# Performance work log

Hardware: AMD Instinct MI355X
Metric: run time of the kernel (lower is better)

The kernel has to match this reference:

```python
import jax, jax.numpy as jnp
import numpy as np

VO, SO, VIN, SM = 16, 100, 16, 100
B, N, K = 2, 8192, 30
EPS = 1e-8

def _split(x, nv):
    v = x[..., :3 * nv].reshape(x.shape[:-1] + (nv, 3))
    s = x[..., 3 * nv:]
    return v, s

def _merge(v, s):
    return jnp.concatenate([v.reshape(v.shape[:-2] + (-1,)), s], axis=-1)

def _vnorm(v):  # [..., nv, 3] -> [..., nv]
    return jnp.sqrt(jnp.sum(v * v, axis=-1) + EPS)

def gvp(x, nv_in, Wh, Wv, Ws, bs, nls=True, nlv=True):
    v, s = _split(x, nv_in)
    vh = jnp.einsum('...ic,ih->...hc', v, Wh)          # vi -> h vector linear
    vn = _vnorm(vh)                                     # rotation-invariant norms
    s_out = jnp.concatenate([s, vn], axis=-1) @ Ws + bs
    if nls:
        s_out = jax.nn.relu(s_out)
    v_out = jnp.einsum('...hc,ho->...oc', vh, Wv)       # h -> vo vector linear
    if nlv:
        v_out = v_out * jax.nn.sigmoid(_vnorm(v_out))[..., None]
    return _merge(v_out, s_out)

def gvp_layernorm(x, nv, g, b):
    v, s = _split(x, nv)
    vn2 = jnp.sum(v * v, axis=-1, keepdims=True)        # [..., nv, 1]
    denom = jnp.sqrt(jnp.mean(vn2, axis=-2, keepdims=True) + EPS)
    v = v / denom
    mu = jnp.mean(s, axis=-1, keepdims=True)
    var = jnp.var(s, axis=-1, keepdims=True)
    s = (s - mu) / jnp.sqrt(var + 1e-5) * g + b
    return _merge(v, s)

def setup_inputs() -> dict:
    key = jax.random.key(0)
    ks = jax.random.split(key, 24)
    def W(i, shape):
        return jax.random.normal(ks[i], shape, dtype=jnp.float32) / np.float32(np.sqrt(shape[0]))
    d = {}
    d['h_V'] = jax.random.normal(ks[0], (B, N, 3 * VO + SO), dtype=jnp.float32)
    d['h_M'] = jax.random.normal(ks[1], (B, N, K, 3 * VIN + SM), dtype=jnp.float32)
    d['mask_V'] = jax.random.randint(ks[2], (B, N), 0, 2, dtype=jnp.int32)
    d['mask_attend'] = jax.random.randint(ks[3], (B, N, K), 0, 2, dtype=jnp.int32)
    # W_EV: GVP(vi=32,si=200,vo=16,so=100,h=32) -> GVP(16,100,16,100) -> GVP(16,100,16,100,no nl)
    d['Wh1'] = W(4, (32, 32)); d['Wv1'] = W(5, (32, 16)); d['Ws1'] = W(6, (232, 100)); d['bs1'] = jnp.zeros((100,), jnp.float32)
    d['Wh2'] = W(7, (16, 16)); d['Wv2'] = W(8, (16, 16)); d['Ws2'] = W(9, (116, 100)); d['bs2'] = jnp.zeros((100,), jnp.float32)
    d['Wh3'] = W(10, (16, 16)); d['Wv3'] = W(11, (16, 16)); d['Ws3'] = W(12, (116, 100)); d['bs3'] = jnp.zeros((100,), jnp.float32)
    # W_dh: GVP(vi=16,si=100,vo=32,so=400,h=32) -> GVP(vi=32,si=400,vo=16,so=100,h=32,no nl)
    d['Wh4'] = W(13, (16, 32)); d['Wv4'] = W(14, (32, 32)); d['Ws4'] = W(15, (132, 400)); d['bs4'] = jnp.zeros((400,), jnp.float32)
    d['Wh5'] = W(16, (32, 32)); d['Wv5'] = W(17, (32, 16)); d['Ws5'] = W(18, (432, 100)); d['bs5'] = jnp.zeros((100,), jnp.float32)
    d['ln0_g'] = jnp.ones((SO,), jnp.float32); d['ln0_b'] = jnp.zeros((SO,), jnp.float32)
    d['ln1_g'] = jnp.ones((SO,), jnp.float32); d['ln1_b'] = jnp.zeros((SO,), jnp.float32)
    return d

def reference(h_V, h_M, mask_V, mask_attend,
              Wh1, Wv1, Ws1, bs1, Wh2, Wv2, Ws2, bs2, Wh3, Wv3, Ws3, bs3,
              Wh4, Wv4, Ws4, bs4, Wh5, Wv5, Ws5, bs5,
              ln0_g, ln0_b, ln1_g, ln1_b):
    # expand node features over neighbor axis and vs_concat with messages
    hVe = jnp.broadcast_to(h_V[:, :, None, :], (B, N, K, h_V.shape[-1]))
    vV, sV = _split(hVe, VO)
    vM, sM = _split(h_M, VIN)
    h_EV = _merge(jnp.concatenate([vV, vM], axis=-2), jnp.concatenate([sV, sM], axis=-1))
    m = gvp(h_EV, VO + VIN, Wh1, Wv1, Ws1, bs1)
    m = gvp(m, VO, Wh2, Wv2, Ws2, bs2)
    m = gvp(m, VO, Wh3, Wv3, Ws3, bs3, nls=False, nlv=False)
    m = mask_attend[..., None].astype(jnp.float32) * m
    dh = jnp.mean(m, axis=2)
    h = gvp_layernorm(h_V + dh, VO, ln0_g, ln0_b)  # dropout rate 0 -> identity
    dh2 = gvp(h, VO, Wh4, Wv4, Ws4, bs4)
    dh2 = gvp(dh2, 2 * VO, Wh5, Wv5, Ws5, bs5, nls=False, nlv=False)
    h = gvp_layernorm(h + dh2, VO, ln1_g, ln1_b)
    h = mask_V[..., None].astype(jnp.float32) * h
    return h
```

## Files before the change

kernel.cpp:

```cpp
#include <hip/hip_runtime.h>

#define KK 30
#define F 148
#define NNODE 16384

typedef short bf16x8 __attribute__((ext_vector_type(8)));
typedef float f32x4v __attribute__((ext_vector_type(4)));

__device__ __forceinline__ ushort f2bf(float x) {
  unsigned u = __float_as_uint(x);
  unsigned r = (u + 0x7FFF + ((u >> 16) & 1)) >> 16;
  return (ushort)r;
}
__device__ __forceinline__ float bf2f(ushort b) { return __uint_as_float(((unsigned)b) << 16); }
__device__ __forceinline__ unsigned pk2(float x, float y) {
  return (unsigned)f2bf(x) | ((unsigned)f2bf(y) << 16);
}
__device__ __forceinline__ void bsplit(float x, ushort& h, ushort& l) {
  ushort hh = f2bf(x); h = hh; l = f2bf(x - bf2f(hh));
}

#define WS_S1B 0
#define WS_VHB (NNODE * 100)
#define WS_WSB (NNODE * 100 + NNODE * 96)
#define B1HI 0
#define B1LO 17920
#define B2HI 35840
#define B2LO 50176
#define B3HI 64512
#define B3LO 78848

__global__ void prep_weights(const float* __restrict__ Ws1, const float* __restrict__ Ws2,
                             const float* __restrict__ Ws3, ushort* __restrict__ ws) {
  int i = blockIdx.x * 256 + threadIdx.x;
  if (i < 17920) {
    int n = i / 160, k = i % 160;
    float w = (n < 100 && k < 132) ? Ws1[(100 + k) * 100 + n] : 0.f;
    ushort h, l; bsplit(w, h, l);
    ws[B1HI + i] = h; ws[B1LO + i] = l;
  } else if (i < 17920 + 14336) {
    int j = i - 17920; int n = j / 128, k = j % 128;
    float w = (n < 100 && k < 116) ? Ws2[k * 100 + n] : 0.f;
    ushort h, l; bsplit(w, h, l);
    ws[B2HI + j] = h; ws[B2LO + j] = l;
  } else if (i < 17920 + 2 * 14336) {
    int j = i - 17920 - 14336; int n = j / 128, k = j % 128;
    float w = (n < 100 && k < 116) ? Ws3[k * 100 + n] : 0.f;
    ushort h, l; bsplit(w, h, l);
    ws[B3HI + j] = h; ws[B3LO + j] = l;
  }
}

__global__ __launch_bounds__(192)
void prep_node(const float* __restrict__ h_V, const float* __restrict__ Ws1,
               const float* __restrict__ bs1, const float* __restrict__ Wh1,
               float* __restrict__ s1bg, float* __restrict__ vhbg) {
  __shared__ float sv[148];
  const int node = blockIdx.x, tid = threadIdx.x;
  for (int f = tid; f < F; f += 192) sv[f] = h_V[(long)node * F + f];
  __syncthreads();
  if (tid < 100) {
    float acc = bs1[tid];
#pragma unroll 4
    for (int i = 0; i < 100; i++) acc = fmaf(sv[48 + i], Ws1[i * 100 + tid], acc);
    s1bg[node * 100 + tid] = acc;
  } else if (tid < 132) {
    int h = tid - 100;
    float a0 = 0.f, a1 = 0.f, a2 = 0.f;
#pragma unroll 4
    for (int i = 0; i < 16; i++) {
      float w = Wh1[i * 32 + h];
      a0 = fmaf(sv[3*i], w, a0); a1 = fmaf(sv[3*i+1], w, a1); a2 = fmaf(sv[3*i+2], w, a2);
    }
    vhbg[node * 96 + 3*h + 0] = a0;
    vhbg[node * 96 + 3*h + 1] = a1;
    vhbg[node * 96 + 3*h + 2] = a2;
  }
}

#define DECL12 float a00=0,a01=0,a02=0,a10=0,a11=0,a12=0,a20=0,a21=0,a22=0,a30=0,a31=0,a32=0;
#define FMA3x4(v0_,v1_,v2_,w_) \
  a00=fmaf(v0_,w_.x,a00); a01=fmaf(v1_,w_.x,a01); a02=fmaf(v2_,w_.x,a02); \
  a10=fmaf(v0_,w_.y,a10); a11=fmaf(v1_,w_.y,a11); a12=fmaf(v2_,w_.y,a12); \
  a20=fmaf(v0_,w_.z,a20); a21=fmaf(v1_,w_.z,a21); a22=fmaf(v2_,w_.z,a22); \
  a30=fmaf(v0_,w_.w,a30); a31=fmaf(v1_,w_.w,a31); a32=fmaf(v2_,w_.w,a32);

#define GATE3(x0,x1,x2,d0,d1,d2) { float vn_=sqrtf((x0)*(x0)+(x1)*(x1)+(x2)*(x2)+1e-8f); \
  float g_=1.f/(1.f+expf(-vn_)); d0=(x0)*g_; d1=(x1)*g_; d2=(x2)*g_; }

template<int NI, bool GATEF>
__device__ __forceinline__ void vtaskb(const unsigned* __restrict__ vsrc,
                                       const float* __restrict__ wbase, int wstride,
                                       float* __restrict__ vdst)
{
  DECL12
#pragma unroll 4
  for (int h2 = 0; h2 < NI / 2; h2++) {
    unsigned d0 = vsrc[3*h2+0], d1 = vsrc[3*h2+1], d2 = vsrc[3*h2+2];
    float4 w0 = *(const float4*)(wbase + (2*h2) * wstride);
    float4 w1 = *(const float4*)(wbase + (2*h2+1) * wstride);
    float e0 = bf2f((ushort)d0), e1 = bf2f((ushort)(d0 >> 16)), e2 = bf2f((ushort)d1);
    float g0 = bf2f((ushort)(d1 >> 16)), g1 = bf2f((ushort)d2), g2 = bf2f((ushort)(d2 >> 16));
    FMA3x4(e0, e1, e2, w0)
    FMA3x4(g0, g1, g2, w1)
  }
  if (GATEF) {
    GATE3(a00,a01,a02, vdst[0],vdst[1],vdst[2])
    GATE3(a10,a11,a12, vdst[3],vdst[4],vdst[5])
    GATE3(a20,a21,a22, vdst[6],vdst[7],vdst[8])
    GATE3(a30,a31,a32, vdst[9],vdst[10],vdst[11])
  } else {
    vdst[0]=a00; vdst[1]=a01; vdst[2]=a02;  vdst[3]=a10; vdst[4]=a11; vdst[5]=a12;
    vdst[6]=a20; vdst[7]=a21; vdst[8]=a22;  vdst[9]=a30; vdst[10]=a31; vdst[11]=a32;
  }
}

template<int NI>
__device__ __forceinline__ void vhtaskb(const float* __restrict__ vsrc,
                                        const float* __restrict__ wbase, int wstride,
                                        unsigned* __restrict__ vdst_u, ushort* __restrict__ ncol)
{
  DECL12
#pragma unroll 4
  for (int h = 0; h < NI; h++) {
    float v0 = vsrc[3*h], v1 = vsrc[3*h+1], v2 = vsrc[3*h+2];
    float4 w = *(const float4*)(wbase + h * wstride);
    FMA3x4(v0, v1, v2, w)
  }
  vdst_u[0] = pk2(a00,a01); vdst_u[1] = pk2(a02,a10); vdst_u[2] = pk2(a11,a12);
  vdst_u[3] = pk2(a20,a21); vdst_u[4] = pk2(a22,a30); vdst_u[5] = pk2(a31,a32);
  float n0 = sqrtf(a00*a00+a01*a01+a02*a02 + 1e-8f);
  float n1 = sqrtf(a10*a10+a11*a11+a12*a12 + 1e-8f);
  float n2 = sqrtf(a20*a20+a21*a21+a22*a22 + 1e-8f);
  float n3 = sqrtf(a30*a30+a31*a31+a32*a32 + 1e-8f);
  unsigned* p = (unsigned*)ncol;
  p[0] = pk2(n0, n1); p[1] = pk2(n2, n3);
}

template<int NKS>
__device__ __forceinline__ void mfma_nt2(const ushort* __restrict__ A, int astr,
                                         const ushort* __restrict__ B_hi,
                                         const ushort* __restrict__ B_lo,
                                         int lane, f32x4v& c0, f32x4v& c1)
{
  int r = lane & 15, q = lane >> 4;
  const int ka = q * 8;
#pragma unroll
  for (int ks = 0; ks < NKS; ks++) {
    int ko = ka + ks * 32;
    bf16x8 a0 = *(const bf16x8*)(A + r * astr + ko);
    bf16x8 a1 = *(const bf16x8*)(A + (16 + r) * astr + ko);
    bf16x8 bh = *(const bf16x8*)(B_hi + ko);
    bf16x8 bl = *(const bf16x8*)(B_lo + ko);
    c0 = __builtin_amdgcn_mfma_f32_16x16x32_bf16(a0, bh, c0, 0, 0, 0);
    c0 = __builtin_amdgcn_mfma_f32_16x16x32_bf16(a0, bl, c0, 0, 0, 0);
    c1 = __builtin_amdgcn_mfma_f32_16x16x32_bf16(a1, bh, c1, 0, 0, 0);
    c1 = __builtin_amdgcn_mfma_f32_16x16x32_bf16(a1, bl, c1, 0, 0, 0);
  }
}

#define P_SV   0
#define P_MKB  148
#define P_VA   152
#define P_VB   1624
#define P_DH   3064
#define P_A2   3164
#define P_A    5340
#define A1S 160
#define A2S 136
#define POOL_F 7900

__global__ __launch_bounds__(256, 5)
void mpnn_fused(const float* __restrict__ h_V, const float* __restrict__ h_M,
                const int* __restrict__ mask_V, const int* __restrict__ mask_attend,
                const float* __restrict__ Wh1, const float* __restrict__ Wv1,
                const float* __restrict__ Wv2, const float* __restrict__ bs2,
                const float* __restrict__ Wv3, const float* __restrict__ bs3,
                const float* __restrict__ Wh2, const float* __restrict__ Wh3,
                const float* __restrict__ Wh4, const float* __restrict__ Wv4,
                const float* __restrict__ Ws4, const float* __restrict__ bs4,
                const float* __restrict__ Wh5, const float* __restrict__ Wv5,
                const float* __restrict__ Ws5, const float* __restrict__ bs5,
                const float* __restrict__ ln0_g, const float* __restrict__ ln0_b,
                const float* __restrict__ ln1_g, const float* __restrict__ ln1_b,
                const float* __restrict__ s1bg, const float* __restrict__ vhbg,
                const ushort* __restrict__ wsb,
                float* __restrict__ out)
{
  __shared__ float pool[POOL_F];
  float* sv   = pool + P_SV;
  float* VAp  = pool + P_VA;
  ushort* VBu = (ushort*)(pool + P_VB);
  float* dhs  = pool + P_DH;
  ushort* A1 = (ushort*)(pool + P_A);
  ushort* A2 = (ushort*)(pool + P_A2);

  const int tid = threadIdx.x;
  const int node = blockIdx.x;
  const int wave = tid >> 6, lane = tid & 63;

  for (int f = tid; f < F; f += 256) sv[f] = h_V[(long)node * F + f];
  {
    unsigned long long bal = __ballot(tid < KK && mask_attend[node * KK + tid] != 0);
    if (tid == 0) *(unsigned*)(pool + P_MKB) = (unsigned)bal;
  }
  for (int t = tid; t < 448; t += 256) {
    int r = t / 14, c2 = t % 14;
    ((unsigned*)A1)[((r * A1S + 132) >> 1) + c2] = 0;
  }
  for (int t = tid; t < 192; t += 256) {
    int r = t / 6, c2 = t % 6;
    ((unsigned*)A2)[((r * A2S + 116) >> 1) + c2] = 0;
  }
  for (int task = tid; task < KK * 37; task += 256) {
    int k = task / 37, q = task % 37;
    float4 d = *(const float4*)(h_M + ((long)node * KK + k) * F + q * 4);
    if (q < 12) {
      VAp[k * 49 + q * 4 + 0] = d.x; VAp[k * 49 + q * 4 + 1] = d.y;
      VAp[k * 49 + q * 4 + 2] = d.z; VAp[k * 49 + q * 4 + 3] = d.w;
    } else {
      int j0 = q * 4 - 48;
      unsigned* p = (unsigned*)(A1 + k * A1S + j0);
      p[0] = (unsigned)f2bf(d.x) | ((unsigned)f2bf(d.y) << 16);
      p[1] = (unsigned)f2bf(d.z) | ((unsigned)f2bf(d.w) << 16);
    }
  }
  __syncthreads();

  if (tid < 240) {
    int k = tid >> 3, h0 = (tid & 7) * 4;
    const float4* vb4 = (const float4*)(vhbg + (long)node * 96 + 3 * h0);
    float4 q0 = vb4[0], q1 = vb4[1], q2 = vb4[2];
    float a00=q0.x,a01=q0.y,a02=q0.z, a10=q0.w,a11=q1.x,a12=q1.y,
          a20=q1.z,a21=q1.w,a22=q2.x, a30=q2.y,a31=q2.z,a32=q2.w;
#pragma unroll 4
    for (int i = 0; i < 16; i++) {
      float v0 = VAp[k*49+3*i], v1 = VAp[k*49+3*i+1], v2 = VAp[k*49+3*i+2];
      float4 w = *(const float4*)(Wh1 + (16 + i) * 32 + h0);
      FMA3x4(v0, v1, v2, w)
    }
    unsigned* vb = (unsigned*)(VBu + k * 96 + 3 * h0);
    vb[0]=pk2(a00,a01); vb[1]=pk2(a02,a10); vb[2]=pk2(a11,a12);
    vb[3]=pk2(a20,a21); vb[4]=pk2(a22,a30); vb[5]=pk2(a31,a32);
    float n0 = sqrtf(a00*a00+a01*a01+a02*a02 + 1e-8f);
    float n1 = sqrtf(a10*a10+a11*a11+a12*a12 + 1e-8f);
    float n2 = sqrtf(a20*a20+a21*a21+a22*a22 + 1e-8f);
    float n3 = sqrtf(a30*a30+a31*a31+a32*a32 + 1e-8f);
    unsigned* p = (unsigned*)(A1 + k * A1S + 100 + h0);
    p[0] = pk2(n0, n1); p[1] = pk2(n2, n3);
  }
  __syncthreads();

  if (wave < 2) {
    int r = lane & 15, q = lane >> 4;
    int nt0 = (wave == 0) ? 0 : 4, nt1 = (wave == 0) ? 4 : 7;
    for (int nt = nt0; nt < nt1; nt++) {
      int n = nt * 16 + r;
      float base = (n < 100) ? s1bg[(long)node * 100 + n] : 0.f;
      f32x4v c0 = {0,0,0,0}, c1 = {0,0,0,0};
      mfma_nt2<5>(A1, A1S, wsb + B1HI + n * 160, wsb + B1LO + n * 160, lane, c0, c1);
      unsigned* dst = (unsigned*)A2;
#pragma unroll
      for (int reg = 0; reg < 4; reg++) {
        int m0 = q * 4 + reg, m1 = m0 + 16;
        unsigned hx = f2bf(fmaxf(c0[reg] + base, 0.f));
        unsigned ox = __shfl_down(hx, 1);
        unsigned hy = f2bf(fmaxf(c1[reg] + base, 0.f));
        unsigned oy = __shfl_down(hy, 1);
        if (((lane & 1) == 0) && n < 100) {
          dst[(m0 * A2S + n) >> 1] = hx | (ox << 16);
          if (m1 < 30) dst[(m1 * A2S + n) >> 1] = hy | (oy << 16);
        }
      }
    }
  } else {
    int vt = tid - 128;
    if (vt < 120) { int k = vt >> 2, o0 = (vt & 3) * 4;
      vtaskb<32, true>((const unsigned*)(VBu + k * 96), Wv1 + o0, 16, VAp + k*49 + 3*o0); }
  }
  __syncthreads();

  if (tid < 120) {
    int k = tid >> 2, h0 = (tid & 3) * 4;
    vhtaskb<16>(VAp + k*49, Wh2 + h0, 16,
                (unsigned*)(VBu + k*96 + 3*h0), A2 + k*A2S + 100 + h0);
  }
  __syncthreads();

  if (wave < 2) {
    int r = lane & 15, q = lane >> 4;
    int nt0 = (wave == 0) ? 0 : 4, nt1 = (wave == 0) ? 4 : 7;
    for (int nt = nt0; nt < nt1; nt++) {
      f32x4v c0 = {0,0,0,0}, c1 = {0,0,0,0};
      int n = nt * 16 + r;
      mfma_nt2<4>(A2, A2S, wsb + B2HI + n * 128, wsb + B2LO + n * 128, lane, c0, c1);
      float base = (n < 100) ? bs2[n] : 0.f;
      unsigned* dst = (unsigned*)A1;
#pragma unroll
      for (int reg = 0; reg < 4; reg++) {
        int m0 = q * 4 + reg, m1 = m0 + 16;
        unsigned hx = f2bf(fmaxf(c0[reg] + base, 0.f));
        unsigned ox = __shfl_down(hx, 1);
        unsigned hy = f2bf(fmaxf(c1[reg] + base, 0.f));
        unsigned oy = __shfl_down(hy, 1);
        if (((lane & 1) == 0) && n < 100) {
          dst[(m0 * A1S + n) >> 1] = hx | (ox << 16);
          if (m1 < 30) dst[(m1 * A1S + n) >> 1] = hy | (oy << 16);
        }
      }
    }
  } else {
    int vt = tid - 128;
    if (vt < 120) { int k = vt >> 2, o0 = (vt & 3) * 4;
      vtaskb<16, true>((const unsigned*)(VBu + k * 96), Wv2 + o0, 16, VAp + k*49 + 3*o0); }
  }
  __syncthreads();

  if (tid < 120) {
    int k = tid >> 2, h0 = (tid & 3) * 4;
    vhtaskb<16>(VAp + k*49, Wh3 + h0, 16,
                (unsigned*)(VBu + k*96 + 3*h0), A1 + k*A1S + 100 + h0);
  } else if (tid >= 240) {
    for (int t = tid - 240; t < 192; t += 16) {
      int r = t / 6, c2 = t % 6;
      ((unsigned*)A1)[((r * A1S + 116) >> 1) + c2] = 0;
    }
  }
  __syncthreads();

  if (wave < 2) {
    unsigned mkb = *(unsigned*)(pool + P_MKB);
    int r = lane & 15, q = lane >> 4;
    int nt0 = (wave == 0) ? 0 : 4, nt1 = (wave == 0) ? 4 : 7;
    for (int nt = nt0; nt < nt1; nt++) {
      f32x4v c0 = {0,0,0,0}, c1 = {0,0,0,0};
      int n = nt * 16 + r;
      mfma_nt2<4>(A1, A1S, wsb + B3HI + n * 128, wsb + B3LO + n * 128, lane, c0, c1);
      float part = 0.f;
#pragma unroll
      for (int reg = 0; reg < 4; reg++) {
        int m0 = q * 4 + reg, m1 = m0 + 16;
        part += ((mkb >> m0) & 1) ? c0[reg] : 0.f;
        part += ((mkb >> m1) & 1) ? c1[reg] : 0.f;
      }
      part += __shfl_xor(part, 16);
      part += __shfl_xor(part, 32);
      if (q == 0 && n < 100) dhs[n] = part;
    }
  } else {
    int vt = tid - 128;
    if (vt < 120) { int k = vt >> 2, o0 = (vt & 3) * 4;
      vtaskb<16, false>((const unsigned*)(VBu + k * 96), Wv3 + o0, 16, VAp + k*49 + 3*o0); }
  }
  __syncthreads();

  float* ns   = pool + P_A;
  float* xb   = ns;
  float* hb   = ns + 160;
  float* nvh4 = ns + 320;
  float* nvn4 = ns + 416;
  float* s4   = ns + 448;
  float* nvn5 = ns + 848;
  float* v4   = ns + 880;
  float* nvh5 = ns + 976;
  float* v5   = ns + 1072;
  float* s5   = ns + 1120;
  float* red  = ns + 1220;
  float* part = ns + 1232;

  {
    unsigned mkb = *(unsigned*)(pool + P_MKB);
    float cntf = (float)__popc(mkb);
    for (int f = tid; f < F; f += 256) {
      float acc;
      if (f < 48) { acc = 0.f; for (int k = 0; k < KK; k++) if ((mkb >> k) & 1) acc += VAp[k*49 + f]; }
      else        { int j = f - 48; acc = dhs[j] + cntf * bs3[j]; }
      xb[f] = sv[f] + acc * (1.f / (float)KK);
    }
  }
  __syncthreads();
  if (tid < 64) {
    float a = (tid < 50) ? xb[48 + 2 * tid] : 0.f;
    float b = (tid < 50) ? xb[48 + 2 * tid + 1] : 0.f;
    float s = a + b, qq = a * a + b * b;
    for (int off = 32; off; off >>= 1) { s += __shfl_down(s, off); qq += __shfl_down(qq, off); }
    if (tid == 0) { red[1] = s * 0.01f; red[2] = qq * 0.01f; }
  } else if (tid < 128) {
    int l = tid - 64;
    float v = (l < 48) ? xb[l] : 0.f;
    float qq = v * v;
    for (int off = 32; off; off >>= 1) qq += __shfl_down(qq, off);
    if (l == 0) red[0] = sqrtf(qq * (1.f / 16.f) + 1e-8f);
  }
  __syncthreads();
  {
    float denom = red[0], mu = red[1];
    float var = red[2] - mu * mu;
    float rs = rsqrtf(var + 1e-5f);
    for (int f = tid; f < F; f += 256) {
      if (f < 48) hb[f] = xb[f] / denom;
      else { int j = f - 48; hb[f] = (xb[f] - mu) * rs * ln0_g[j] + ln0_b[j]; }
    }
  }
  __syncthreads();

  if (tid < 32) {
    int h = tid;
    float a0 = 0.f, a1 = 0.f, a2 = 0.f;
#pragma unroll 4
    for (int i = 0; i < 16; i++) {
      float w = Wh4[i * 32 + h];
      a0 = fmaf(hb[3*i], w, a0); a1 = fmaf(hb[3*i+1], w, a1); a2 = fmaf(hb[3*i+2], w, a2);
    }
    nvh4[3*h] = a0; nvh4[3*h+1] = a1; nvh4[3*h+2] = a2;
    nvn4[h] = sqrtf(a0*a0 + a1*a1 + a2*a2 + 1e-8f);
  }
  __syncthreads();
  if (tid < 200) {
    int j0 = tid * 2;
    float ax = bs4[j0], ay = bs4[j0 + 1];
    const float* w = Ws4 + j0;
#pragma unroll 4
    for (int i = 0; i < 100; i++) {
      float s = hb[48 + i];
      float2 w2 = *(const float2*)(w + i * 400);
      ax = fmaf(s, w2.x, ax); ay = fmaf(s, w2.y, ay);
    }
#pragma unroll 4
    for (int h = 0; h < 32; h++) {
      float s = nvn4[h];
      float2 w2 = *(const float2*)(w + (100 + h) * 400);
      ax = fmaf(s, w2.x, ax); ay = fmaf(s, w2.y, ay);
    }
    s4[j0] = fmaxf(ax, 0.f); s4[j0 + 1] = fmaxf(ay, 0.f);
  } else if (tid >= 224) {
    int o = tid - 224;
    float a0 = 0.f, a1 = 0.f, a2 = 0.f;
#pragma unroll 4
    for (int h = 0; h < 32; h++) {
      float w = Wv4[h * 32 + o];
      a0 = fmaf(nvh4[3*h], w, a0); a1 = fmaf(nvh4[3*h+1], w, a1); a2 = fmaf(nvh4[3*h+2], w, a2);
    }
    GATE3(a0, a1, a2, v4[3*o], v4[3*o+1], v4[3*o+2])
  }
  __syncthreads();
  if (tid < 32) {
    int h = tid;
    float a0 = 0.f, a1 = 0.f, a2 = 0.f;
#pragma unroll 4
    for (int i = 0; i < 32; i++) {
      float w = Wh5[i * 32 + h];
      a0 = fmaf(v4[3*i], w, a0); a1 = fmaf(v4[3*i+1], w, a1); a2 = fmaf(v4[3*i+2], w, a2);
    }
    nvh5[3*h] = a0; nvh5[3*h+1] = a1; nvh5[3*h+2] = a2;
    nvn5[h] = sqrtf(a0*a0 + a1*a1 + a2*a2 + 1e-8f);
  }
  __syncthreads();
  if (tid < 200) {
    int jq = tid / 8, c = tid % 8, j0 = jq * 4;
    int ibeg = c * 54, iend = ibeg + 54;
    float4 acc = make_float4(0.f, 0.f, 0.f, 0.f);
    const float* w = Ws5 + j0;
#pragma unroll 4
    for (int i = ibeg; i < iend; i++) {
      float s = s4[i];
      float4 w4 = *(const float4*)(w + i * 100);
      acc.x = fmaf(s, w4.x, acc.x); acc.y = fmaf(s, w4.y, acc.y);
      acc.z = fmaf(s, w4.z, acc.z); acc.w = fmaf(s, w4.w, acc.w);
    }
    *(float4*)&part[tid * 4] = acc;
  } else if (tid >= 224 && tid < 240) {
    int o = tid - 224;
    float a0 = 0.f, a1 = 0.f, a2 = 0.f;
#pragma unroll 4
    for (int h = 0; h < 32; h++) {
      float w = Wv5[h * 16 + o];
      a0 = fmaf(nvh5[3*h], w, a0); a1 = fmaf(nvh5[3*h+1], w, a1); a2 = fmaf(nvh5[3*h+2], w, a2);
    }
    v5[3*o] = a0; v5[3*o+1] = a1; v5[3*o+2] = a2;
  }
  __syncthreads();
  if (tid < 25) {
    int j0 = tid * 4;
    float4 b = *(const float4*)(bs5 + j0);
    float4 acc = b;
#pragma unroll
    for (int c = 0; c < 8; c++) {
      float4 p = *(const float4*)&part[(tid * 8 + c) * 4];
      acc.x += p.x; acc.y += p.y; acc.z += p.z; acc.w += p.w;
    }
    *(float4*)&s5[j0] = acc;
  }
  __syncthreads();
  for (int f = tid; f < F; f += 256) {
    float d = (f < 48) ? v5[f] : s5[f - 48];
    xb[f] = hb[f] + d;
  }
  __syncthreads();
  if (tid < 64) {
    float a = (tid < 50) ? xb[48 + 2 * tid] : 0.f;
    float b = (tid < 50) ? xb[48 + 2 * tid + 1] : 0.f;
    float s = a + b, qq = a * a + b * b;
    for (int off = 32; off; off >>= 1) { s += __shfl_down(s, off); qq += __shfl_down(qq, off); }
    if (tid == 0) { red[1] = s * 0.01f; red[2] = qq * 0.01f; }
  } else if (tid < 128) {
    int l = tid - 64;
    float v = (l < 48) ? xb[l] : 0.f;
    float qq = v * v;
    for (int off = 32; off; off >>= 1) qq += __shfl_down(qq, off);
    if (l == 0) red[0] = sqrtf(qq * (1.f / 16.f) + 1e-8f);
  }
  __syncthreads();
  {
    float denom = red[0], mu = red[1];
    float var = red[2] - mu * mu;
    float rs = rsqrtf(var + 1e-5f);
    float mv = (float)mask_V[node];
    for (int f = tid; f < F; f += 256) {
      float val;
      if (f < 48) val = xb[f] / denom;
      else { int j = f - 48; val = (xb[f] - mu) * rs * ln1_g[j] + ln1_b[j]; }
      out[(long)node * F + f] = mv * val;
    }
  }
}

extern "C" void kernel_launch(void* const* d_in, const int* in_sizes, int n_in,
                              void* d_out, int out_size, void* d_ws, size_t ws_size,
                              hipStream_t stream) {
  const float* h_V  = (const float*)d_in[0];
  const float* h_M  = (const float*)d_in[1];
  const int* mask_V = (const int*)d_in[2];
  const int* mask_attend = (const int*)d_in[3];
  const float* Wh1 = (const float*)d_in[4];
  const float* Wv1 = (const float*)d_in[5];
  const float* Ws1 = (const float*)d_in[6];
  const float* bs1 = (const float*)d_in[7];
  const float* Wh2 = (const float*)d_in[8];
  const float* Wv2 = (const float*)d_in[9];
  const float* Ws2 = (const float*)d_in[10];
  const float* bs2 = (const float*)d_in[11];
  const float* Wh3 = (const float*)d_in[12];
  const float* Wv3 = (const float*)d_in[13];
  const float* Ws3 = (const float*)d_in[14];
  const float* bs3 = (const float*)d_in[15];
  const float* Wh4 = (const float*)d_in[16];
  const float* Wv4 = (const float*)d_in[17];
  const float* Ws4 = (const float*)d_in[18];
  const float* bs4 = (const float*)d_in[19];
  const float* Wh5 = (const float*)d_in[20];
  const float* Wv5 = (const float*)d_in[21];
  const float* Ws5 = (const float*)d_in[22];
  const float* bs5 = (const float*)d_in[23];
  const float* ln0_g = (const float*)d_in[24];
  const float* ln0_b = (const float*)d_in[25];
  const float* ln1_g = (const float*)d_in[26];
  const float* ln1_b = (const float*)d_in[27];
  float* out = (float*)d_out;

  float* wsf = (float*)d_ws;
  float* s1bg = wsf + WS_S1B;
  float* vhbg = wsf + WS_VHB;
  ushort* wsb = (ushort*)(wsf + WS_WSB);

  prep_weights<<<dim3(182), dim3(256), 0, stream>>>(Ws1, Ws2, Ws3, wsb);
  prep_node<<<dim3(NNODE), dim3(192), 0, stream>>>(h_V, Ws1, bs1, Wh1, s1bg, vhbg);
  mpnn_fused<<<dim3(NNODE), dim3(256), 0, stream>>>(
      h_V, h_M, mask_V, mask_attend,
      Wh1, Wv1, Wv2, bs2, Wv3, bs3, Wh2, Wh3,
      Wh4, Wv4, Ws4, bs4, Wh5, Wv5, Ws5, bs5,
      ln0_g, ln0_b, ln1_g, ln1_b, s1bg, vhbg, wsb, out);
}
```

Before: 1.334 ms.

## Batch prep_node over 16 nodes and fuse vector gate with next vh linear

prep_node now handles 16 nodes per block and stages a transposed Ws1 and Wh1 in shared memory, so weight reads are amortised across nodes. In mpnn_fused the gated vector linear and the following Wh linear are merged into one per-thread routine that swaps gated vectors between the four lanes of a row with shuffles. This removes the fp32 VA staging round-trip and one __syncthreads per GVP layer. The shared-memory layout is reshuffled to fit, and a few unroll factors are raised, at the cost of more registers and shuffle traffic.

Measured after the change: 1.375 ms. 3.1% more time.

```diff
diff --git a/kernel.cpp b/kernel.cpp
--- a/kernel.cpp
+++ b/kernel.cpp
@@ -3,6 +3,7 @@
 #define KK 30
 #define F 148
 #define NNODE 16384
+#define NPB 16
 
 typedef short bf16x8 __attribute__((ext_vector_type(8)));
 typedef float f32x4v __attribute__((ext_vector_type(4)));
@@ -51,30 +52,46 @@
   }
 }
 
-__global__ __launch_bounds__(192)
+__global__ __launch_bounds__(256)
 void prep_node(const float* __restrict__ h_V, const float* __restrict__ Ws1,
                const float* __restrict__ bs1, const float* __restrict__ Wh1,
                float* __restrict__ s1bg, float* __restrict__ vhbg) {
-  __shared__ float sv[148];
-  const int node = blockIdx.x, tid = threadIdx.x;
-  for (int f = tid; f < F; f += 192) sv[f] = h_V[(long)node * F + f];
-  __syncthreads();
-  if (tid < 100) {
-    float acc = bs1[tid];
-#pragma unroll 4
-    for (int i = 0; i < 100; i++) acc = fmaf(sv[48 + i], Ws1[i * 100 + tid], acc);
-    s1bg[node * 100 + tid] = acc;
-  } else if (tid < 132) {
-    int h = tid - 100;
+  __shared__ float wt[100 * 101];
+  __shared__ float wh[512];
+  __shared__ float svs[NPB * 148];
+  const int tid = threadIdx.x;
+  const long node0 = (long)blockIdx.x * NPB;
+  for (int idx = tid; idx < 10000; idx += 256) {
+    int i = idx / 100, n = idx - i * 100;
+    wt[n * 101 + i] = Ws1[idx];
+  }
+  for (int idx = tid; idx < 512; idx += 256) wh[idx] = Wh1[idx];
+  for (int idx = tid; idx < NPB * 148; idx += 256) {
+    int nd = idx / 148, f = idx - nd * 148;
+    svs[idx] = h_V[(node0 + nd) * 148 + f];
+  }
+  __syncthreads();
+  for (int task = tid; task < NPB * 100; task += 256) {
+    int nd = task / 100, n = task - nd * 100;
+    const float* s = svs + nd * 148 + 48;
+    const float* w = wt + n * 101;
+    float acc = bs1[n];
+#pragma unroll 10
+    for (int i = 0; i < 100; i++) acc = fmaf(s[i], w[i], acc);
+    s1bg[(node0 + nd) * 100 + n] = acc;
+  }
+  for (int task = tid; task < NPB * 32; task += 256) {
+    int nd = task >> 5, h = task & 31;
+    const float* s = svs + nd * 148;
     float a0 = 0.f, a1 = 0.f, a2 = 0.f;
 #pragma unroll 4
     for (int i = 0; i < 16; i++) {
-      float w = Wh1[i * 32 + h];
-      a0 = fmaf(sv[3*i], w, a0); a1 = fmaf(sv[3*i+1], w, a1); a2 = fmaf(sv[3*i+2], w, a2);
-    }
-    vhbg[node * 96 + 3*h + 0] = a0;
-    vhbg[node * 96 + 3*h + 1] = a1;
-    vhbg[node * 96 + 3*h + 2] = a2;
+      float w = wh[i * 32 + h];
+      a0 = fmaf(s[3*i], w, a0); a1 = fmaf(s[3*i+1], w, a1); a2 = fmaf(s[3*i+2], w, a2);
+    }
+    vhbg[(node0 + nd) * 96 + 3*h + 0] = a0;
+    vhbg[(node0 + nd) * 96 + 3*h + 1] = a1;
+    vhbg[(node0 + nd) * 96 + 3*h + 2] = a2;
   }
 }
 
@@ -116,19 +133,44 @@
 }
 
 template<int NI>
-__device__ __forceinline__ void vhtaskb(const float* __restrict__ vsrc,
-                                        const float* __restrict__ wbase, int wstride,
-                                        unsigned* __restrict__ vdst_u, ushort* __restrict__ ncol)
+__device__ __forceinline__ void v_vh_fused(const unsigned* vsrc,
+                                           const float* __restrict__ Wv,
+                                           const float* __restrict__ Whn,
+                                           int c, int h0,
+                                           unsigned* vrow_u, ushort* ncol)
 {
   DECL12
-#pragma unroll 4
-  for (int h = 0; h < NI; h++) {
-    float v0 = vsrc[3*h], v1 = vsrc[3*h+1], v2 = vsrc[3*h+2];
-    float4 w = *(const float4*)(wbase + h * wstride);
-    FMA3x4(v0, v1, v2, w)
-  }
-  vdst_u[0] = pk2(a00,a01); vdst_u[1] = pk2(a02,a10); vdst_u[2] = pk2(a11,a12);
-  vdst_u[3] = pk2(a20,a21); vdst_u[4] = pk2(a22,a30); vdst_u[5] = pk2(a31,a32);
+#pragma unroll
+  for (int h2 = 0; h2 < NI / 2; h2++) {
+    unsigned d0 = vsrc[3*h2+0], d1 = vsrc[3*h2+1], d2 = vsrc[3*h2+2];
+    float4 w0 = *(const float4*)(Wv + (2*h2) * 16);
+    float4 w1 = *(const float4*)(Wv + (2*h2+1) * 16);
+    float e0 = bf2f((ushort)d0), e1 = bf2f((ushort)(d0 >> 16)), e2 = bf2f((ushort)d1);
+    float f0 = bf2f((ushort)(d1 >> 16)), f1 = bf2f((ushort)d2), f2 = bf2f((ushort)(d2 >> 16));
+    FMA3x4(e0, e1, e2, w0)
+    FMA3x4(f0, f1, f2, w1)
+  }
+  float gg[12];
+  GATE3(a00,a01,a02, gg[0],gg[1],gg[2])
+  GATE3(a10,a11,a12, gg[3],gg[4],gg[5])
+  GATE3(a20,a21,a22, gg[6],gg[7],gg[8])
+  GATE3(a30,a31,a32, gg[9],gg[10],gg[11])
+  a00=0;a01=0;a02=0;a10=0;a11=0;a12=0;a20=0;a21=0;a22=0;a30=0;a31=0;a32=0;
+#pragma unroll
+  for (int m = 0; m < 4; m++) {
+    float t[12];
+#pragma unroll
+    for (int z = 0; z < 12; z++) t[z] = (m == 0) ? gg[z] : __shfl_xor(gg[z], m);
+    int ob = (c ^ m) * 4;
+#pragma unroll
+    for (int j = 0; j < 4; j++) {
+      float4 w = *(const float4*)(Whn + (ob + j) * 16 + h0);
+      FMA3x4(t[3*j], t[3*j+1], t[3*j+2], w)
+    }
+  }
+  unsigned* vb = vrow_u + ((3 * h0) >> 1);
+  vb[0]=pk2(a00,a01); vb[1]=pk2(a02,a10); vb[2]=pk2(a11,a12);
+  vb[3]=pk2(a20,a21); vb[4]=pk2(a22,a30); vb[5]=pk2(a31,a32);
   float n0 = sqrtf(a00*a00+a01*a01+a02*a02 + 1e-8f);
   float n1 = sqrtf(a10*a10+a11*a11+a12*a12 + 1e-8f);
   float n2 = sqrtf(a20*a20+a21*a21+a22*a22 + 1e-8f);
@@ -161,14 +203,14 @@
 
 #define P_SV   0
 #define P_MKB  148
-#define P_VA   152
-#define P_VB   1624
-#define P_DH   3064
-#define P_A2   3164
-#define P_A    5340
-#define A1S 160
+#define P_DH   152
+#define P_A2   252
+#define P_A    2292
+#define P_VA   4812
+#define P_VB   6282
+#define A1S 168
 #define A2S 136
-#define POOL_F 7900
+#define POOL_F 7722
 
 __global__ __launch_bounds__(256, 5)
 void mpnn_fused(const float* __restrict__ h_V, const float* __restrict__ h_M,
@@ -189,9 +231,9 @@
 {
   __shared__ float pool[POOL_F];
   float* sv   = pool + P_SV;
+  float* dhs  = pool + P_DH;
   float* VAp  = pool + P_VA;
   ushort* VBu = (ushort*)(pool + P_VB);
-  float* dhs  = pool + P_DH;
   ushort* A1 = (ushort*)(pool + P_A);
   ushort* A2 = (ushort*)(pool + P_A2);
 
@@ -204,13 +246,13 @@
     unsigned long long bal = __ballot(tid < KK && mask_attend[node * KK + tid] != 0);
     if (tid == 0) *(unsigned*)(pool + P_MKB) = (unsigned)bal;
   }
-  for (int t = tid; t < 448; t += 256) {
+  for (int t = tid; t < 420; t += 256) {
     int r = t / 14, c2 = t % 14;
-    ((unsigned*)A1)[((r * A1S + 132) >> 1) + c2] = 0;
-  }
-  for (int t = tid; t < 192; t += 256) {
+    ((unsigned*)A1)[r * 84 + 66 + c2] = 0;
+  }
+  for (int t = tid; t < 180; t += 256) {
     int r = t / 6, c2 = t % 6;
-    ((unsigned*)A2)[((r * A2S + 116) >> 1) + c2] = 0;
+    ((unsigned*)A2)[r * 68 + 58 + c2] = 0;
   }
   for (int task = tid; task < KK * 37; task += 256) {
     int k = task / 37, q = task % 37;
@@ -275,15 +317,11 @@
     }
   } else {
     int vt = tid - 128;
-    if (vt < 120) { int k = vt >> 2, o0 = (vt & 3) * 4;
-      vtaskb<32, true>((const unsigned*)(VBu + k * 96), Wv1 + o0, 16, VAp + k*49 + 3*o0); }
-  }
-  __syncthreads();
-
-  if (tid < 120) {
-    int k = tid >> 2, h0 = (tid & 3) * 4;
-    vhtaskb<16>(VAp + k*49, Wh2 + h0, 16,
-                (unsigned*)(VBu + k*96 + 3*h0), A2 + k*A2S + 100 + h0);
+    if (vt < 120) {
+      int k = vt >> 2, c = vt & 3, h0 = c * 4;
+      v_vh_fused<32>((const unsigned*)(VBu + k * 96), Wv1 + h0, Wh2, c, h0,
+                     (unsigned*)(VBu + k * 96), A2 + k * A2S + 100 + h0);
+    }
   }
   __syncthreads();
 
@@ -311,19 +349,15 @@
     }
   } else {
     int vt = tid - 128;
-    if (vt < 120) { int k = vt >> 2, o0 = (vt & 3) * 4;
-      vtaskb<16, true>((const unsigned*)(VBu + k * 96), Wv2 + o0, 16, VAp + k*49 + 3*o0); }
-  }
-  __syncthreads();
-
-  if (tid < 120) {
-    int k = tid >> 2, h0 = (tid & 3) * 4;
-    vhtaskb<16>(VAp + k*49, Wh3 + h0, 16,
-                (unsigned*)(VBu + k*96 + 3*h0), A1 + k*A1S + 100 + h0);
-  } else if (tid >= 240) {
-    for (int t = tid - 240; t < 192; t += 16) {
-      int r = t / 6, c2 = t % 6;
-      ((unsigned*)A1)[((r * A1S + 116) >> 1) + c2] = 0;
+    if (vt < 120) {
+      int k = vt >> 2, c = vt & 3, h0 = c * 4;
+      v_vh_fused<16>((const unsigned*)(VBu + k * 96), Wv2 + h0, Wh3, c, h0,
+                     (unsigned*)(VBu + k * 96), A1 + k * A1S + 100 + h0);
+    } else {
+      for (int t = vt - 120; t < 180; t += 8) {
+        int r = t / 6, c2 = t % 6;
+        ((unsigned*)A1)[r * 84 + 58 + c2] = 0;
+      }
     }
   }
   __syncthreads();
@@ -420,13 +454,13 @@
     int j0 = tid * 2;
     float ax = bs4[j0], ay = bs4[j0 + 1];
     const float* w = Ws4 + j0;
-#pragma unroll 4
+#pragma unroll 10
     for (int i = 0; i < 100; i++) {
       float s = hb[48 + i];
       float2 w2 = *(const float2*)(w + i * 400);
       ax = fmaf(s, w2.x, ax); ay = fmaf(s, w2.y, ay);
     }
-#pragma unroll 4
+#pragma unroll 8
     for (int h = 0; h < 32; h++) {
       float s = nvn4[h];
       float2 w2 = *(const float2*)(w + (100 + h) * 400);
@@ -461,7 +495,7 @@
     int ibeg = c * 54, iend = ibeg + 54;
     float4 acc = make_float4(0.f, 0.f, 0.f, 0.f);
     const float* w = Ws5 + j0;
-#pragma unroll 4
+#pragma unroll 6
     for (int i = ibeg; i < iend; i++) {
       float s = s4[i];
       float4 w4 = *(const float4*)(w + i * 100);
@@ -564,7 +598,7 @@
   ushort* wsb = (ushort*)(wsf + WS_WSB);
 
   prep_weights<<<dim3(182), dim3(256), 0, stream>>>(Ws1, Ws2, Ws3, wsb);
-  prep_node<<<dim3(NNODE), dim3(192), 0, stream>>>(h_V, Ws1, bs1, Wh1, s1bg, vhbg);
+  prep_node<<<dim3(NNODE / NPB), dim3(256), 0, stream>>>(h_V, Ws1, bs1, Wh1, s1bg, vhbg);
   mpnn_fused<<<dim3(NNODE), dim3(256), 0, stream>>>(
       h_V, h_M, mask_V, mask_attend,
       Wh1, Wv1, Wv2, bs2, Wv3, bs3, Wh2, Wh3,
```
